# Performance work log

Measured on AMD Instinct MI355X. Metric: run time of the kernel, lower is better.

Reference implementation:

```python
import jax, jax.numpy as jnp
import numpy as np

N = 100000   # nodes
E = 1600000  # edges
G = 64       # graphs in batch
DIMS = [(7, 128), (128, 128), (128, 256)]
EPS = 1e-5


def setup_inputs() -> dict:
    key = jax.random.key(0)
    ks = jax.random.split(key, 32)
    inp = {}
    inp["x"] = jax.random.normal(ks[0], (N, 7), dtype=jnp.float32)
    inp["edge_index"] = jax.random.randint(ks[1], (2, E), 0, N, dtype=jnp.int64)
    inp["batch"] = jnp.sort(jax.random.randint(ks[2], (N,), 0, G, dtype=jnp.int64))
    ki = 3
    for i, (din, dout) in enumerate(DIMS):
        inp[f"Wl{i}"] = jax.random.normal(ks[ki], (din, dout), dtype=jnp.float32) * 0.05; ki += 1
        inp[f"bl{i}"] = jnp.zeros((dout,), dtype=jnp.float32)
        inp[f"Wr{i}"] = jax.random.normal(ks[ki], (din, dout), dtype=jnp.float32) * 0.05; ki += 1
        inp[f"g{i}"] = jax.random.uniform(ks[ki], (dout,), dtype=jnp.float32) + 0.5; ki += 1
        inp[f"be{i}"] = jax.random.normal(ks[ki], (dout,), dtype=jnp.float32) * 0.1; ki += 1
        inp[f"rm{i}"] = jax.random.normal(ks[ki], (dout,), dtype=jnp.float32) * 0.1; ki += 1
        inp[f"rv{i}"] = jax.random.uniform(ks[ki], (dout,), dtype=jnp.float32) + 0.5; ki += 1
    return inp


def _sage(x, src, dst, Wl, bl, Wr):
    # mean-aggregate neighbor features: out[i] = mean_{(j->i)} x[j]
    agg = jax.ops.segment_sum(x[src], dst, num_segments=N)          # [N, din]
    cnt = jax.ops.segment_sum(jnp.ones((src.shape[0],), x.dtype), dst, num_segments=N)
    mean = agg / jnp.maximum(cnt, 1.0)[:, None]
    return x @ Wl + bl + mean @ Wr


def _bn_relu(x, g, be, rm, rv):
    # BatchNorm1d in eval mode (running stats) + ReLU; dropout is a no-op in eval
    return jax.nn.relu((x - rm) * jax.lax.rsqrt(rv + EPS) * g + be)


def reference(x, edge_index, batch,
              Wl0, bl0, Wr0, g0, be0, rm0, rv0,
              Wl1, bl1, Wr1, g1, be1, rm1, rv1,
              Wl2, bl2, Wr2, g2, be2, rm2, rv2):
    src, dst = edge_index[0], edge_index[1]
    layers = [(Wl0, bl0, Wr0, g0, be0, rm0, rv0),
              (Wl1, bl1, Wr1, g1, be1, rm1, rv1),
              (Wl2, bl2, Wr2, g2, be2, rm2, rv2)]
    for Wl, bl, Wr, g, be, rm, rv in layers:
        x = _sage(x, src, dst, Wl, bl, Wr)
        x = _bn_relu(x, g, be, rm, rv)
    pooled = jax.ops.segment_sum(x, batch, num_segments=G)  # global_add_pool
    return (pooled, x)
```

## Files before the change

kernel.cpp:

```cpp
#include <hip/hip_runtime.h>
#include <hip/hip_bf16.h>

#define EPSV 1e-5f
#define PSHIFT 6
#define PMASK 63
#define PCAP 1536
#define B1SHIFT 11
#define B1MASK ((1 << B1SHIFT) - 1)
#define B1CAP 34816
#define SPLIT 16

typedef __attribute__((ext_vector_type(8))) short bf16x8;
typedef __attribute__((ext_vector_type(4))) float f32x4;
typedef __attribute__((ext_vector_type(4))) unsigned u32x4;

__device__ __forceinline__ float bf2f(unsigned short u) {
    unsigned x = ((unsigned)u) << 16;
    return __builtin_bit_cast(float, x);
}
__device__ __forceinline__ unsigned short f2bf(float f) {
    unsigned x = __builtin_bit_cast(unsigned, f);
    unsigned r = (x + 0x7fffu + ((x >> 16) & 1u)) >> 16;
    return (unsigned short)r;
}
__device__ __forceinline__ float u32lo(unsigned v) {
    return __builtin_bit_cast(float, v << 16);
}
__device__ __forceinline__ float u32hi(unsigned v) {
    return __builtin_bit_cast(float, v & 0xffff0000u);
}
__device__ __forceinline__ f32x4 bflo4(u32x4 v) {
    f32x4 r;
    r.x = __builtin_bit_cast(float, v.x << 16);
    r.y = __builtin_bit_cast(float, v.y << 16);
    r.z = __builtin_bit_cast(float, v.z << 16);
    r.w = __builtin_bit_cast(float, v.w << 16);
    return r;
}
__device__ __forceinline__ f32x4 bfhi4(u32x4 v) {
    f32x4 r;
    r.x = __builtin_bit_cast(float, v.x & 0xffff0000u);
    r.y = __builtin_bit_cast(float, v.y & 0xffff0000u);
    r.z = __builtin_bit_cast(float, v.z & 0xffff0000u);
    r.w = __builtin_bit_cast(float, v.w & 0xffff0000u);
    return r;
}


__global__ __launch_bounds__(256) void k_scatter1(const int* __restrict__ src,
                                                  const int* __restrict__ dst,
                                                  int* __restrict__ bcnt1,
                                                  unsigned* __restrict__ stg1,
                                                  int E, int NB1) {
    __shared__ int hist[64], sbase[64], scur[64];
    int t = threadIdx.x;
    int base = blockIdx.x * 2048;
    if (t < 64) { hist[t] = 0; scur[t] = 0; }
    __syncthreads();
    unsigned val[8];
    int cb[8];
#pragma unroll
    for (int k = 0; k < 8; k++) {
        int i = base + k * 256 + t;
        if (i < E) {
            int d = __builtin_nontemporal_load(&dst[i]);
            int s = __builtin_nontemporal_load(&src[i]);
            cb[k] = d >> B1SHIFT;
            val[k] = ((unsigned)s << B1SHIFT) | (unsigned)(d & B1MASK);
            atomicAdd(&hist[cb[k]], 1);
        } else
            cb[k] = -1;
    }
    __syncthreads();
    if (t < NB1 && hist[t] > 0) sbase[t] = atomicAdd(&bcnt1[t], hist[t]);
    __syncthreads();
#pragma unroll
    for (int k = 0; k < 8; k++) {
        if (cb[k] >= 0) {
            int r = atomicAdd(&scur[cb[k]], 1);
            int slot = sbase[cb[k]] + r;
            if (slot < B1CAP) stg1[(size_t)cb[k] * B1CAP + slot] = val[k];
        }
    }
}

__global__ __launch_bounds__(256) void k_scatter2(const int* __restrict__ bcnt1,
                                                  const unsigned* __restrict__ stg1,
                                                  int* __restrict__ pcnt,
                                                  unsigned* __restrict__ pstg) {
    __shared__ int hist[32], sbase[32], scur[32];
    int cb = blockIdx.x >> 4;
    int sl = blockIdx.x & (SPLIT - 1);
    int t = threadIdx.x;
    if (t < 32) { hist[t] = 0; scur[t] = 0; }
    int cnt = min(bcnt1[cb], B1CAP);
    int per = (cnt + SPLIT - 1) / SPLIT;
    int lo = sl * per, hi = min(lo + per, cnt);
    __syncthreads();
    const unsigned* sp = stg1 + (size_t)cb * B1CAP;
    for (int j = lo + t; j < hi; j += 256)
        atomicAdd(&hist[(sp[j] >> 6) & 31], 1);
    __syncthreads();
    if (t < 32 && hist[t] > 0) sbase[t] = atomicAdd(&pcnt[(cb << 5) + t], hist[t]);
    __syncthreads();
    for (int j = lo + t; j < hi; j += 256) {
        unsigned v = sp[j];
        int pr = (v >> 6) & 31;
        int r = atomicAdd(&scur[pr], 1);
        int slot = sbase[pr] + r;
        if (slot < PCAP)
            pstg[(size_t)((cb << 5) + pr) * PCAP + slot] =
                ((v >> 5) & ~63u) | (v & 63u);
    }
}

__global__ __launch_bounds__(256) void k_meta(const int* __restrict__ pcnt,
                                              int* __restrict__ pbase,
                                              int* __restrict__ off,
                                              const int* __restrict__ batch,
                                              int* __restrict__ gstart,
                                              int NPART, int Nn, int G) {
    if (blockIdx.x == 1) {
        int g = threadIdx.x;
        if (g > G) return;
        if (g == G) {
            gstart[G] = Nn;
            return;
        }
        int lo = 0, hi = Nn;
        while (lo < hi) {
            int mid = (lo + hi) >> 1;
            if (batch[mid] < g) lo = mid + 1;
            else hi = mid;
        }
        gstart[g] = lo;
        return;
    }
    __shared__ int red[256];
    int t = threadIdx.x;
    int chunk = (NPART + 255) / 256;
    int lo = t * chunk, hi = min(lo + chunk, NPART);
    int s = 0;
    for (int p = lo; p < hi; p++) {
        int tt = min(pcnt[p], PCAP);
        pbase[p] = tt;
        s += tt;
    }
    red[t] = s;
    __syncthreads();
    for (int d = 1; d < 256; d <<= 1) {
        int v = (t >= d) ? red[t - d] : 0;
        __syncthreads();
        red[t] += v;
        __syncthreads();
    }
    int base = (t == 0) ? 0 : red[t - 1];
    for (int p = lo; p < hi; p++) {
        int tt = pbase[p];
        pbase[p] = base;
        base += tt;
    }
    if (t == 255) off[Nn] = red[255];
}

__global__ __launch_bounds__(256) void k_build(const int* __restrict__ pcnt,
                                               const unsigned* __restrict__ pstg,
                                               const int* __restrict__ pbase,
                                               int* __restrict__ off,
                                               int* __restrict__ csr, int Nn) {
    __shared__ unsigned ed[PCAP];
    __shared__ int srt[PCAP];
    __shared__ int cnt[64], loff[64], cur[64];
    int p = blockIdx.x, t = threadIdx.x;
    int tot = min(pcnt[p], PCAP);
    if (t < 64) cnt[t] = 0;
    __syncthreads();
    const unsigned* sp = pstg + (size_t)p * PCAP;
    for (int j = t; j < tot; j += 256) {
        unsigned e = __builtin_nontemporal_load(&sp[j]);
        ed[j] = e;
        atomicAdd(&cnt[e & PMASK], 1);
    }
    __syncthreads();
    if (t == 0) {
        int a = 0;
        for (int j = 0; j < 64; j++) {
            loff[j] = a;
            cur[j] = a;
            a += cnt[j];
        }
    }
    __syncthreads();
    int base = pbase[p];
    int node0 = p << PSHIFT;
    if (t < 64 && node0 + t < Nn) off[node0 + t] = base + loff[t];
    for (int j = t; j < tot; j += 256) {
        unsigned e = ed[j];
        int pos = atomicAdd(&cur[e & PMASK], 1);
        srt[pos] = (int)(e >> PSHIFT);
    }
    __syncthreads();
    for (int j = t; j < tot; j += 256) csr[base + j] = srt[j];
}


__global__ __launch_bounds__(256) void k_prepx(const float* __restrict__ x,
                                               unsigned short* __restrict__ x7b,
                                               int n) {
    int u = blockIdx.x * 256 + threadIdx.x;
    if (u >= n * 8) return;
    int node = u >> 3, f = u & 7;
    float v = (f < 7) ? x[(size_t)node * 7 + f] : 0.f;
    x7b[u] = f2bf(v);
}


__global__ __launch_bounds__(256) void k_agg7(const unsigned* __restrict__ x7b,
                                              const int* __restrict__ off,
                                              const int* __restrict__ csr,
                                              float* __restrict__ mean, int n) {
    int i = (blockIdx.x * 256 + threadIdx.x) >> 2;
    int r = threadIdx.x & 3;
    if (i >= n) return;
    int a = off[i], b = off[i + 1];
    float a0 = 0.f, a1 = 0.f;
    int j = a;
    for (; j + 3 < b; j += 4) {
        unsigned v0 = x7b[(size_t)csr[j] * 4 + r];
        unsigned v1 = x7b[(size_t)csr[j + 1] * 4 + r];
        unsigned v2 = x7b[(size_t)csr[j + 2] * 4 + r];
        unsigned v3 = x7b[(size_t)csr[j + 3] * 4 + r];
        a0 += u32lo(v0) + u32lo(v1) + u32lo(v2) + u32lo(v3);
        a1 += u32hi(v0) + u32hi(v1) + u32hi(v2) + u32hi(v3);
    }
    for (; j < b; j++) {
        unsigned v = x7b[(size_t)csr[j] * 4 + r];
        a0 += u32lo(v);
        a1 += u32hi(v);
    }
    float inv = 1.0f / (float)max(b - a, 1);
    *(float2*)&mean[(size_t)i * 8 + r * 2] = make_float2(a0 * inv, a1 * inv);
}

__global__ __launch_bounds__(256) void k_agg128(const unsigned short* __restrict__ x,
                                                const int* __restrict__ off,
                                                const int* __restrict__ csr,
                                                unsigned short* __restrict__ mean,
                                                int n) {
    int q = (blockIdx.x * 256 + threadIdx.x) >> 4;
    int sl = threadIdx.x & 15;
    if (q >= n) return;
    int a = off[q], b = off[q + 1];
    const u32x4* xr = (const u32x4*)x;
    f32x4 aL = {0.f, 0.f, 0.f, 0.f}, aH = {0.f, 0.f, 0.f, 0.f};
    int j = a;
    for (; j + 3 < b; j += 4) {
        int s0 = csr[j], s1 = csr[j + 1], s2 = csr[j + 2], s3 = csr[j + 3];
        u32x4 v0 = xr[(size_t)s0 * 16 + sl];
        u32x4 v1 = xr[(size_t)s1 * 16 + sl];
        u32x4 v2 = xr[(size_t)s2 * 16 + sl];
        u32x4 v3 = xr[(size_t)s3 * 16 + sl];
        aL += bflo4(v0) + bflo4(v1) + bflo4(v2) + bflo4(v3);
        aH += bfhi4(v0) + bfhi4(v1) + bfhi4(v2) + bfhi4(v3);
    }
    for (; j < b; j++) {
        u32x4 v = xr[(size_t)csr[j] * 16 + sl];
        aL += bflo4(v);
        aH += bfhi4(v);
    }
    float inv = 1.0f / (float)max(b - a, 1);
    u32x4 o;
    o.x = (unsigned)f2bf(aL.x * inv) | ((unsigned)f2bf(aH.x * inv) << 16);
    o.y = (unsigned)f2bf(aL.y * inv) | ((unsigned)f2bf(aH.y * inv) << 16);
    o.z = (unsigned)f2bf(aL.z * inv) | ((unsigned)f2bf(aH.z * inv) << 16);
    o.w = (unsigned)f2bf(aL.w * inv) | ((unsigned)f2bf(aH.w * inv) << 16);
    *((u32x4*)mean + (size_t)q * 16 + sl) = o;
}


__global__ __launch_bounds__(256) void k_prepw_all(
    const float* __restrict__ Wl1, const float* __restrict__ Wr1,
    const float* __restrict__ Wl2, const float* __restrict__ Wr2,
    unsigned short* __restrict__ Wlt1, unsigned short* __restrict__ Wrt1,
    unsigned short* __restrict__ Wlt2, unsigned short* __restrict__ Wrt2) {
    int u = blockIdx.x * 256 + threadIdx.x;
    const float* W;
    unsigned short* Wt;
    int Ncols, v;
    if (u < 32768) {
        v = u & 16383;
        W = (u < 16384) ? Wl1 : Wr1;
        Wt = (u < 16384) ? Wlt1 : Wrt1;
        Ncols = 128;
    } else {
        v = (u - 32768) & 32767;
        W = (u < 65536) ? Wl2 : Wr2;
        Wt = (u < 65536) ? Wlt2 : Wrt2;
        Ncols = 256;
    }
    int n = v % Ncols, k = v / Ncols;
    Wt[(size_t)n * 128 + k] = f2bf(W[(size_t)k * Ncols + n]);
}


__global__ __launch_bounds__(256) void k_layer0(
    const float* __restrict__ x, const float* __restrict__ mean,
    const float* __restrict__ Wl, const float* __restrict__ bl,
    const float* __restrict__ Wr, const float* __restrict__ g,
    const float* __restrict__ be, const float* __restrict__ rm,
    const float* __restrict__ rv, unsigned short* __restrict__ out, int n) {
    __shared__ float xs[32][8];
    __shared__ float ms[32][8];
    int tid = threadIdx.x;
    int col = tid & 127;
    int hr = tid >> 7;
    int row0 = blockIdx.x * 32;

    float wl[7], wr[7];
#pragma unroll
    for (int k = 0; k < 7; k++) {
        wl[k] = Wl[k * 128 + col];
        wr[k] = Wr[k * 128 + col];
    }
    float sc = g[col] * rsqrtf(rv[col] + EPSV);
    float sh = (bl[col] - rm[col]) * sc + be[col];

    if (tid < 224) {
        int r = tid / 7, f = tid % 7;
        int gr = row0 + r;
        xs[r][f] = (gr < n) ? x[(size_t)gr * 7 + f] : 0.f;
    }
    {
        int r = tid >> 3, f = tid & 7;
        int gr = row0 + r;
        ms[r][f] = (gr < n) ? mean[(size_t)gr * 8 + f] : 0.f;
    }
    __syncthreads();

#pragma unroll
    for (int rr = 0; rr < 16; rr++) {
        int r = hr * 16 + rr;
        int grow = row0 + r;
        if (grow >= n) break;
        float acc = 0.f;
#pragma unroll
        for (int k = 0; k < 7; k++) acc = fmaf(xs[r][k], wl[k], acc);
#pragma unroll
        for (int k = 0; k < 7; k++) acc = fmaf(ms[r][k], wr[k], acc);
        float h = acc * sc + sh;
        out[(size_t)grow * 128 + col] = f2bf(fmaxf(h, 0.f));
    }
}


template <int COLS, int DOUT, bool BF16OUT>
__global__ __launch_bounds__(256) void k_mfma_layer(
    const unsigned short* __restrict__ xin, const unsigned short* __restrict__ meanb,
    const unsigned short* __restrict__ Wlt, const unsigned short* __restrict__ Wrt,
    const float* __restrict__ bl, const float* __restrict__ g,
    const float* __restrict__ be, const float* __restrict__ rm,
    const float* __restrict__ rv, void* __restrict__ outv, int n) {
    __shared__ unsigned short As[64 * 40];
    __shared__ unsigned short Bs[COLS * 40];

    int tid = threadIdx.x;
    int wave = tid >> 6;
    int lane = tid & 63;
    int m = lane & 15;
    int half = lane >> 4;
    int row0 = blockIdx.x * 64;
    int colbase = blockIdx.y * COLS;

    const int NCB = COLS / 16;
    f32x4 acc[NCB] = {};

    for (int s = 0; s < 8; s++) {
        int pass = s >> 2;
        int k0 = (s & 3) * 32;
        const unsigned short* Asrc = pass ? meanb : xin;
        const unsigned short* Wt = pass ? Wrt : Wlt;

        __syncthreads();
        {
            int rr = tid >> 2;
            int ks = (tid & 3) * 8;
            int grow = row0 + rr;
            float4 v = make_float4(0.f, 0.f, 0.f, 0.f);
            if (grow < n) v = *(const float4*)&Asrc[(size_t)grow * 128 + k0 + ks];
            *(float4*)&As[rr * 40 + ks] = v;
        }
#pragma unroll
        for (int rep = 0; rep < COLS / 64; rep++) {
            int u = tid + rep * 256;
            int nn = u >> 2;
            int ks = (u & 3) * 8;
            float4 v = *(const float4*)&Wt[(size_t)(colbase + nn) * 128 + k0 + ks];
            *(float4*)&Bs[nn * 40 + ks] = v;
        }
        __syncthreads();

        bf16x8 a = *(const bf16x8*)&As[(wave * 16 + m) * 40 + half * 8];
#pragma unroll
        for (int cb = 0; cb < NCB; cb++) {
            bf16x8 b = *(const bf16x8*)&Bs[(cb * 16 + m) * 40 + half * 8];
            acc[cb] = __builtin_amdgcn_mfma_f32_16x16x32_bf16(a, b, acc[cb], 0, 0, 0);
        }
    }

    float* outf = (float*)outv;
    unsigned short* outb = (unsigned short*)outv;
#pragma unroll
    for (int cb = 0; cb < NCB; cb++) {
        int col = colbase + cb * 16 + m;
        float sc = g[col] * rsqrtf(rv[col] + EPSV);
        float sh = (bl[col] - rm[col]) * sc + be[col];
#pragma unroll
        for (int reg = 0; reg < 4; reg++) {
            int r0 = row0 + wave * 16 + half * 4 + reg;
            if (r0 < n) {
                float h = fmaxf(acc[cb][reg] * sc + sh, 0.f);
                if (BF16OUT) outb[(size_t)r0 * DOUT + col] = f2bf(h);
                else outf[(size_t)r0 * DOUT + col] = h;
            }
        }
    }
}


__global__ __launch_bounds__(256) void k_pool(const float* __restrict__ x3,
                                              const int* __restrict__ gstart,
                                              float* __restrict__ pooled, int G) {
    const int S = 16;
    int g = blockIdx.x / S;
    int s = blockIdx.x % S;
    int a = gstart[g], b = gstart[g + 1];
    int col = threadIdx.x;
    float acc = 0.f;
    for (int r = a + s; r < b; r += S) acc += x3[(size_t)r * 256 + col];
    atomicAdd(&pooled[g * 256 + col], acc);
}


extern "C" void kernel_launch(void* const* d_in, const int* in_sizes, int n_in,
                              void* d_out, int out_size, void* d_ws, size_t ws_size,
                              hipStream_t stream) {
    const float* x = (const float*)d_in[0];
    const int* ei = (const int*)d_in[1];
    const int* batch = (const int*)d_in[2];
    const int N = in_sizes[0] / 7;
    const int E = in_sizes[1] / 2;
    const int G = 64;
    const int* src = ei;
    const int* dst = ei + E;
    const int NPART = (N + PMASK) >> PSHIFT;
    const int NB1 = (N + (1 << B1SHIFT) - 1) >> B1SHIFT;
    const int NBX = (N + 63) / 64;

    const float* P[21];
    for (int i = 0; i < 21; i++) P[i] = (const float*)d_in[3 + i];
    const float **L0 = P, **L1 = P + 7, **L2 = P + 14;

    char* w = (char*)d_ws;
    auto carve = [&](size_t bytes) {
        void* p = (void*)w;
        w += (bytes + 255) & ~(size_t)255;
        return p;
    };
    int* cnts = (int*)carve((size_t)(64 + NPART) * 4);
    int* bcnt1 = cnts;
    int* pcnt = cnts + 64;
    unsigned* stg1 = (unsigned*)carve((size_t)NB1 * B1CAP * 4);
    unsigned* pstg = (unsigned*)carve((size_t)NPART * PCAP * 4);
    int* pbase = (int*)carve((size_t)NPART * 4);
    int* off = (int*)carve(((size_t)N + 1) * 4);
    int* gstart = (int*)carve(((size_t)G + 1) * 4);
    unsigned short* x7b = (unsigned short*)carve((size_t)N * 8 * 2);
    float* mean7 = (float*)carve((size_t)N * 8 * 4);
    unsigned short* x1 = (unsigned short*)carve((size_t)N * 128 * 2);
    unsigned short* meanb = (unsigned short*)carve((size_t)N * 128 * 2);
    unsigned short* Wlt1 = (unsigned short*)carve((size_t)128 * 128 * 2);
    unsigned short* Wrt1 = (unsigned short*)carve((size_t)128 * 128 * 2);
    unsigned short* Wlt2 = (unsigned short*)carve((size_t)128 * 256 * 2);
    unsigned short* Wrt2 = (unsigned short*)carve((size_t)128 * 256 * 2);
    int* csr = (int*)stg1;

    float* pooled = (float*)d_out;
    float* x3 = (float*)d_out + (size_t)G * 256;

    hipMemsetAsync(cnts, 0, (size_t)(64 + NPART) * 4, stream);
    hipMemsetAsync(pooled, 0, (size_t)G * 256 * 4, stream);

    k_scatter1<<<(E + 2047) / 2048, 256, 0, stream>>>(src, dst, bcnt1, stg1, E, NB1);
    k_scatter2<<<NB1 * SPLIT, 256, 0, stream>>>(bcnt1, stg1, pcnt, pstg);
    k_meta<<<2, 256, 0, stream>>>(pcnt, pbase, off, batch, gstart, NPART, N, G);
    k_build<<<NPART, 256, 0, stream>>>(pcnt, pstg, pbase, off, csr, N);
    k_prepx<<<(N * 8 + 255) / 256, 256, 0, stream>>>(x, x7b, N);
    k_prepw_all<<<(98304 + 255) / 256, 256, 0, stream>>>(L1[0], L1[2], L2[0], L2[2],
                                                         Wlt1, Wrt1, Wlt2, Wrt2);

    k_agg7<<<((size_t)N * 4 + 255) / 256, 256, 0, stream>>>((const unsigned*)x7b,
                                                            off, csr, mean7, N);
    k_layer0<<<(N + 31) / 32, 256, 0, stream>>>(x, mean7, L0[0], L0[1], L0[2], L0[3],
                                                L0[4], L0[5], L0[6], x1, N);

    k_agg128<<<((size_t)N * 16 + 255) / 256, 256, 0, stream>>>(x1, off, csr, meanb, N);
    k_mfma_layer<128, 128, true><<<dim3(NBX, 1), 256, 0, stream>>>(
        x1, meanb, Wlt1, Wrt1, L1[1], L1[3], L1[4], L1[5], L1[6], x1, N);

    k_agg128<<<((size_t)N * 16 + 255) / 256, 256, 0, stream>>>(x1, off, csr, meanb, N);
    k_mfma_layer<128, 256, false><<<dim3(NBX, 2), 256, 0, stream>>>(
        x1, meanb, Wlt2, Wrt2, L2[1], L2[3], L2[4], L2[5], L2[6], x3, N);

    k_pool<<<G * 16, 256, 0, stream>>>(x3, gstart, pooled, G);
}
```

Before: 437.1 us.

## Fuse layer-0 aggregation into layer-0 kernel and merge prep/memset launches

Merges the two memsets, the x bf16 conversion and the weight transposes into one init kernel. The 7-dim neighbor aggregation now runs inside the layer-0 kernel and writes straight to shared memory, which removes the mean7 buffer round trip and one launch. The cost is that only 128 of the 256 threads do the gather inside the fused kernel, so the irregular aggregation runs at lower parallelism per block.

After: 426.7 us. 1.02x faster.

```diff
diff --git a/kernel.cpp b/kernel.cpp
--- a/kernel.cpp
+++ b/kernel.cpp
@@ -44,6 +44,42 @@
     r.z = __builtin_bit_cast(float, v.z & 0xffff0000u);
     r.w = __builtin_bit_cast(float, v.w & 0xffff0000u);
     return r;
+}
+
+
+__global__ __launch_bounds__(256) void k_init(
+    const float* __restrict__ x, unsigned short* __restrict__ x7b,
+    const float* __restrict__ Wl1, const float* __restrict__ Wr1,
+    const float* __restrict__ Wl2, const float* __restrict__ Wr2,
+    unsigned short* __restrict__ Wlt1, unsigned short* __restrict__ Wrt1,
+    unsigned short* __restrict__ Wlt2, unsigned short* __restrict__ Wrt2,
+    int* __restrict__ cnts, int ncnt, float* __restrict__ pooled, int n) {
+    int u = blockIdx.x * 256 + threadIdx.x;
+    if (u < n * 8) {
+        int node = u >> 3, f = u & 7;
+        float v = (f < 7) ? x[(size_t)node * 7 + f] : 0.f;
+        x7b[u] = f2bf(v);
+    }
+    if (u < 98304) {
+        const float* W;
+        unsigned short* Wt;
+        int Ncols, v;
+        if (u < 32768) {
+            v = u & 16383;
+            W = (u < 16384) ? Wl1 : Wr1;
+            Wt = (u < 16384) ? Wlt1 : Wrt1;
+            Ncols = 128;
+        } else {
+            v = (u - 32768) & 32767;
+            W = (u < 65536) ? Wl2 : Wr2;
+            Wt = (u < 65536) ? Wlt2 : Wrt2;
+            Ncols = 256;
+        }
+        int nn = v % Ncols, k = v / Ncols;
+        Wt[(size_t)nn * 128 + k] = f2bf(W[(size_t)k * Ncols + nn]);
+    }
+    if (u < ncnt) cnts[u] = 0;
+    if (u < 16384) pooled[u] = 0.f;
 }
 
 
@@ -204,42 +240,74 @@
 }
 
 
-__global__ __launch_bounds__(256) void k_prepx(const float* __restrict__ x,
-                                               unsigned short* __restrict__ x7b,
-                                               int n) {
-    int u = blockIdx.x * 256 + threadIdx.x;
-    if (u >= n * 8) return;
-    int node = u >> 3, f = u & 7;
-    float v = (f < 7) ? x[(size_t)node * 7 + f] : 0.f;
-    x7b[u] = f2bf(v);
-}
-
-
-__global__ __launch_bounds__(256) void k_agg7(const unsigned* __restrict__ x7b,
-                                              const int* __restrict__ off,
-                                              const int* __restrict__ csr,
-                                              float* __restrict__ mean, int n) {
-    int i = (blockIdx.x * 256 + threadIdx.x) >> 2;
-    int r = threadIdx.x & 3;
-    if (i >= n) return;
-    int a = off[i], b = off[i + 1];
-    float a0 = 0.f, a1 = 0.f;
-    int j = a;
-    for (; j + 3 < b; j += 4) {
-        unsigned v0 = x7b[(size_t)csr[j] * 4 + r];
-        unsigned v1 = x7b[(size_t)csr[j + 1] * 4 + r];
-        unsigned v2 = x7b[(size_t)csr[j + 2] * 4 + r];
-        unsigned v3 = x7b[(size_t)csr[j + 3] * 4 + r];
-        a0 += u32lo(v0) + u32lo(v1) + u32lo(v2) + u32lo(v3);
-        a1 += u32hi(v0) + u32hi(v1) + u32hi(v2) + u32hi(v3);
-    }
-    for (; j < b; j++) {
-        unsigned v = x7b[(size_t)csr[j] * 4 + r];
-        a0 += u32lo(v);
-        a1 += u32hi(v);
-    }
-    float inv = 1.0f / (float)max(b - a, 1);
-    *(float2*)&mean[(size_t)i * 8 + r * 2] = make_float2(a0 * inv, a1 * inv);
+__global__ __launch_bounds__(256) void k_l0fused(
+    const float* __restrict__ x, const unsigned* __restrict__ x7b,
+    const int* __restrict__ off, const int* __restrict__ csr,
+    const float* __restrict__ Wl, const float* __restrict__ bl,
+    const float* __restrict__ Wr, const float* __restrict__ g,
+    const float* __restrict__ be, const float* __restrict__ rm,
+    const float* __restrict__ rv, unsigned short* __restrict__ out, int n) {
+    __shared__ float xs[32][8];
+    __shared__ float ms[32][8];
+    int tid = threadIdx.x;
+    int row0 = blockIdx.x * 32;
+
+    if (tid < 224) {
+        int r = tid / 7, f = tid % 7;
+        int gr = row0 + r;
+        xs[r][f] = (gr < n) ? x[(size_t)gr * 7 + f] : 0.f;
+    }
+    if (tid < 128) {
+        int r = tid >> 2, lane = tid & 3;
+        int grow = row0 + r;
+        float a0 = 0.f, a1 = 0.f, inv = 0.f;
+        if (grow < n) {
+            int a = off[grow], b = off[grow + 1];
+            int j = a;
+            for (; j + 3 < b; j += 4) {
+                unsigned v0 = x7b[(size_t)csr[j] * 4 + lane];
+                unsigned v1 = x7b[(size_t)csr[j + 1] * 4 + lane];
+                unsigned v2 = x7b[(size_t)csr[j + 2] * 4 + lane];
+                unsigned v3 = x7b[(size_t)csr[j + 3] * 4 + lane];
+                a0 += u32lo(v0) + u32lo(v1) + u32lo(v2) + u32lo(v3);
+                a1 += u32hi(v0) + u32hi(v1) + u32hi(v2) + u32hi(v3);
+            }
+            for (; j < b; j++) {
+                unsigned v = x7b[(size_t)csr[j] * 4 + lane];
+                a0 += u32lo(v);
+                a1 += u32hi(v);
+            }
+            inv = 1.0f / (float)max(b - a, 1);
+        }
+        ms[r][lane * 2] = a0 * inv;
+        ms[r][lane * 2 + 1] = a1 * inv;
+    }
+
+    int col = tid & 127;
+    float wl[7], wr[7];
+#pragma unroll
+    for (int k = 0; k < 7; k++) {
+        wl[k] = Wl[k * 128 + col];
+        wr[k] = Wr[k * 128 + col];
+    }
+    float sc = g[col] * rsqrtf(rv[col] + EPSV);
+    float sh = (bl[col] - rm[col]) * sc + be[col];
+    __syncthreads();
+
+    int hr = tid >> 7;
+#pragma unroll
+    for (int rr = 0; rr < 16; rr++) {
+        int r = hr * 16 + rr;
+        int grow = row0 + r;
+        if (grow >= n) break;
+        float acc = 0.f;
+#pragma unroll
+        for (int k = 0; k < 7; k++) acc = fmaf(xs[r][k], wl[k], acc);
+#pragma unroll
+        for (int k = 0; k < 7; k++) acc = fmaf(ms[r][k], wr[k], acc);
+        float h = acc * sc + sh;
+        out[(size_t)grow * 128 + col] = f2bf(fmaxf(h, 0.f));
+    }
 }
 
 __global__ __launch_bounds__(256) void k_agg128(const unsigned short* __restrict__ x,
@@ -278,81 +346,6 @@
 }
 
 
-__global__ __launch_bounds__(256) void k_prepw_all(
-    const float* __restrict__ Wl1, const float* __restrict__ Wr1,
-    const float* __restrict__ Wl2, const float* __restrict__ Wr2,
-    unsigned short* __restrict__ Wlt1, unsigned short* __restrict__ Wrt1,
-    unsigned short* __restrict__ Wlt2, unsigned short* __restrict__ Wrt2) {
-    int u = blockIdx.x * 256 + threadIdx.x;
-    const float* W;
-    unsigned short* Wt;
-    int Ncols, v;
-    if (u < 32768) {
-        v = u & 16383;
-        W = (u < 16384) ? Wl1 : Wr1;
-        Wt = (u < 16384) ? Wlt1 : Wrt1;
-        Ncols = 128;
-    } else {
-        v = (u - 32768) & 32767;
-        W = (u < 65536) ? Wl2 : Wr2;
-        Wt = (u < 65536) ? Wlt2 : Wrt2;
-        Ncols = 256;
-    }
-    int n = v % Ncols, k = v / Ncols;
-    Wt[(size_t)n * 128 + k] = f2bf(W[(size_t)k * Ncols + n]);
-}
-
-
-__global__ __launch_bounds__(256) void k_layer0(
-    const float* __restrict__ x, const float* __restrict__ mean,
-    const float* __restrict__ Wl, const float* __restrict__ bl,
-    const float* __restrict__ Wr, const float* __restrict__ g,
-    const float* __restrict__ be, const float* __restrict__ rm,
-    const float* __restrict__ rv, unsigned short* __restrict__ out, int n) {
-    __shared__ float xs[32][8];
-    __shared__ float ms[32][8];
-    int tid = threadIdx.x;
-    int col = tid & 127;
-    int hr = tid >> 7;
-    int row0 = blockIdx.x * 32;
-
-    float wl[7], wr[7];
-#pragma unroll
-    for (int k = 0; k < 7; k++) {
-        wl[k] = Wl[k * 128 + col];
-        wr[k] = Wr[k * 128 + col];
-    }
-    float sc = g[col] * rsqrtf(rv[col] + EPSV);
-    float sh = (bl[col] - rm[col]) * sc + be[col];
-
-    if (tid < 224) {
-        int r = tid / 7, f = tid % 7;
-        int gr = row0 + r;
-        xs[r][f] = (gr < n) ? x[(size_t)gr * 7 + f] : 0.f;
-    }
-    {
-        int r = tid >> 3, f = tid & 7;
-        int gr = row0 + r;
-        ms[r][f] = (gr < n) ? mean[(size_t)gr * 8 + f] : 0.f;
-    }
-    __syncthreads();
-
-#pragma unroll
-    for (int rr = 0; rr < 16; rr++) {
-        int r = hr * 16 + rr;
-        int grow = row0 + r;
-        if (grow >= n) break;
-        float acc = 0.f;
-#pragma unroll
-        for (int k = 0; k < 7; k++) acc = fmaf(xs[r][k], wl[k], acc);
-#pragma unroll
-        for (int k = 0; k < 7; k++) acc = fmaf(ms[r][k], wr[k], acc);
-        float h = acc * sc + sh;
-        out[(size_t)grow * 128 + col] = f2bf(fmaxf(h, 0.f));
-    }
-}
-
-
 template <int COLS, int DOUT, bool BF16OUT>
 __global__ __launch_bounds__(256) void k_mfma_layer(
     const unsigned short* __restrict__ xin, const unsigned short* __restrict__ meanb,
@@ -475,7 +468,6 @@
     int* off = (int*)carve(((size_t)N + 1) * 4);
     int* gstart = (int*)carve(((size_t)G + 1) * 4);
     unsigned short* x7b = (unsigned short*)carve((size_t)N * 8 * 2);
-    float* mean7 = (float*)carve((size_t)N * 8 * 4);
     unsigned short* x1 = (unsigned short*)carve((size_t)N * 128 * 2);
     unsigned short* meanb = (unsigned short*)carve((size_t)N * 128 * 2);
     unsigned short* Wlt1 = (unsigned short*)carve((size_t)128 * 128 * 2);
@@ -487,21 +479,19 @@
     float* pooled = (float*)d_out;
     float* x3 = (float*)d_out + (size_t)G * 256;
 
-    hipMemsetAsync(cnts, 0, (size_t)(64 + NPART) * 4, stream);
-    hipMemsetAsync(pooled, 0, (size_t)G * 256 * 4, stream);
+    int initN = max(N * 8, 98304);
+    k_init<<<(initN + 255) / 256, 256, 0, stream>>>(
+        x, x7b, L1[0], L1[2], L2[0], L2[2], Wlt1, Wrt1, Wlt2, Wrt2,
+        cnts, 64 + NPART, pooled, N);
 
     k_scatter1<<<(E + 2047) / 2048, 256, 0, stream>>>(src, dst, bcnt1, stg1, E, NB1);
     k_scatter2<<<NB1 * SPLIT, 256, 0, stream>>>(bcnt1, stg1, pcnt, pstg);
     k_meta<<<2, 256, 0, stream>>>(pcnt, pbase, off, batch, gstart, NPART, N, G);
     k_build<<<NPART, 256, 0, stream>>>(pcnt, pstg, pbase, off, csr, N);
-    k_prepx<<<(N * 8 + 255) / 256, 256, 0, stream>>>(x, x7b, N);
-    k_prepw_all<<<(98304 + 255) / 256, 256, 0, stream>>>(L1[0], L1[2], L2[0], L2[2],
-                                                         Wlt1, Wrt1, Wlt2, Wrt2);
-
-    k_agg7<<<((size_t)N * 4 + 255) / 256, 256, 0, stream>>>((const unsigned*)x7b,
-                                                            off, csr, mean7, N);
-    k_layer0<<<(N + 31) / 32, 256, 0, stream>>>(x, mean7, L0[0], L0[1], L0[2], L0[3],
-                                                L0[4], L0[5], L0[6], x1, N);
+
+    k_l0fused<<<(N + 31) / 32, 256, 0, stream>>>(
+        x, (const unsigned*)x7b, off, csr, L0[0], L0[1], L0[2], L0[3],
+        L0[4], L0[5], L0[6], x1, N);
 
     k_agg128<<<((size_t)N * 16 + 255) / 256, 256, 0, stream>>>(x1, off, csr, meanb, N);
     k_mfma_layer<128, 128, true><<<dim3(NBX, 1), 256, 0, stream>>>(
```
